# Optimization experiments

Measured on AMD Instinct MI355X. Metric: run time of the kernel, lower is better.

Reference implementation:

```python
import jax, jax.numpy as jnp
import numpy as np

EMBED_DIM = 584
HEADS = 8
HEAD_SIZE = EMBED_DIM // HEADS  # 73
CTX = 200


def setup_inputs() -> dict:
    key = jax.random.key(0)
    ks = jax.random.split(key, 6)
    B, T = 256, 200
    x = jax.random.normal(ks[0], (B, T, EMBED_DIM), dtype=jnp.float32)
    s = 1.0 / np.sqrt(EMBED_DIM)
    # per-head q/k/v Linear(EMBED_DIM, HEAD_SIZE, bias=False) weights, stacked: [H, hs, E]
    Wq = jax.random.uniform(ks[1], (HEADS, HEAD_SIZE, EMBED_DIM), jnp.float32, -s, s)
    Wk = jax.random.uniform(ks[2], (HEADS, HEAD_SIZE, EMBED_DIM), jnp.float32, -s, s)
    Wv = jax.random.uniform(ks[3], (HEADS, HEAD_SIZE, EMBED_DIM), jnp.float32, -s, s)
    Wo = jax.random.uniform(ks[4], (EMBED_DIM, EMBED_DIM), jnp.float32, -s, s)
    bo = jax.random.uniform(ks[5], (EMBED_DIM,), jnp.float32, -s, s)
    return {"x": x, "Wq": Wq, "Wk": Wk, "Wv": Wv, "Wo": Wo, "bo": bo}


def reference(x, Wq, Wk, Wv, Wo, bo):
    B, T, C = x.shape  # C == EMBED_DIM
    # per-head projections, batched: [B, H, T, hs]
    q = jnp.einsum('bte,hfe->bhtf', x, Wq)
    k = jnp.einsum('bte,hfe->bhtf', x, Wk)
    v = jnp.einsum('bte,hfe->bhtf', x, Wv)
    # NOTE: original scales by EMBED_DIM**-0.5 (C), not head_size**-0.5
    scores = jnp.einsum('bhtf,bhsf->bhts', q, k) * (C ** -0.5)
    causal = jnp.tril(jnp.ones((T, T), dtype=bool))
    scores = jnp.where(causal, scores, -jnp.inf)
    w = jax.nn.softmax(scores, axis=-1)
    out = jnp.einsum('bhts,bhsf->bhtf', w, v)  # [B,H,T,hs]
    out = out.transpose(0, 2, 1, 3).reshape(B, T, C)  # concat heads on last dim
    return out @ Wo.T + bo
```

## Files before the change

### kernel.cpp

```cpp
#include <hip/hip_runtime.h>

typedef __bf16 bf16x8 __attribute__((ext_vector_type(8)));
typedef __bf16 bf16x4 __attribute__((ext_vector_type(4)));
typedef float f32x4 __attribute__((ext_vector_type(4)));

#define EMBED 584
#define KP 608
#define HEADS 8
#define HS 73
#define HSQ 80
#define CTX 200
#define NBATCH 256
#define MROWS 51200
#define NQKV 1752

#define PSS 232

__device__ __forceinline__ void gld_lds16(__bf16* lds, const __bf16* g) {
  __builtin_amdgcn_global_load_lds(
      (const __attribute__((address_space(1))) void*)g,
      (__attribute__((address_space(3))) void*)lds, 16, 0, 0);
}

__global__ __launch_bounds__(256) void cvt_x(const float* __restrict__ x,
                                             __bf16* __restrict__ out) {
  int i = blockIdx.x * 256 + threadIdx.x;
  int r = i / 76, slot = i - r * 76;
  int col = slot * 8;
  bf16x8 o8 = {};
  if (col < EMBED) {
    const float4* s4 = (const float4*)(x + (size_t)r * EMBED + col);
    float4 f0 = s4[0], f1 = s4[1];
    o8[0] = (__bf16)f0.x; o8[1] = (__bf16)f0.y; o8[2] = (__bf16)f0.z; o8[3] = (__bf16)f0.w;
    o8[4] = (__bf16)f1.x; o8[5] = (__bf16)f1.y; o8[6] = (__bf16)f1.z; o8[7] = (__bf16)f1.w;
  }
  *(bf16x8*)(out + (size_t)r * KP + col) = o8;
}

__global__ __launch_bounds__(256) void pack_w(const float* __restrict__ Wq,
                                              const float* __restrict__ Wk,
                                              const float* __restrict__ Wv,
                                              const float* __restrict__ Wo,
                                              __bf16* __restrict__ out) {
  int i = blockIdx.x * 256 + threadIdx.x;
  if (i >= 2336 * 76) return;
  int r = i / 76, slot = i - r * 76;
  int col = slot * 8;
  bf16x8 o8 = {};
  if (col < EMBED) {
    const float* src = r < 584  ? Wq + (size_t)r * EMBED
                     : r < 1168 ? Wk + (size_t)(r - 584) * EMBED
                     : r < 1752 ? Wv + (size_t)(r - 1168) * EMBED
                                : Wo + (size_t)(r - 1752) * EMBED;
    const float4* s4 = (const float4*)(src + col);
    float4 f0 = s4[0], f1 = s4[1];
    o8[0] = (__bf16)f0.x; o8[1] = (__bf16)f0.y; o8[2] = (__bf16)f0.z; o8[3] = (__bf16)f0.w;
    o8[4] = (__bf16)f1.x; o8[5] = (__bf16)f1.y; o8[6] = (__bf16)f1.z; o8[7] = (__bf16)f1.w;
  }
  *(bf16x8*)(out + (size_t)r * KP + col) = o8;
}

__global__ __launch_bounds__(256) void zero_pads(__bf16* __restrict__ qb,
                                                 __bf16* __restrict__ kb,
                                                 __bf16* __restrict__ vb) {
  int bh = blockIdx.x;
  bf16x8 z = {};
  __bf16* qp = qb + (size_t)bh * 16000;
  __bf16* kp = kb + (size_t)bh * 16000;
  __bf16* vp = vb + (size_t)bh * 16000;
  for (int i = threadIdx.x; i < 575; i += 256) {
    if (i < 200)      *(bf16x8*)&qp[i * 80 + 72] = z;
    else if (i < 400) *(bf16x8*)&kp[(i - 200) * 80 + 72] = z;
    else              *(bf16x8*)&vp[14600 + (i - 400) * 8] = z;
  }
}

__global__ __launch_bounds__(256) void gemm_qkv(const __bf16* __restrict__ A,
                                                const __bf16* __restrict__ Bm,
                                                __bf16* __restrict__ Q,
                                                __bf16* __restrict__ Ko,
                                                __bf16* __restrict__ V) {
  __shared__ __bf16 As[3][4096];
  __shared__ __bf16 Bs[3][4096];
  int tid = threadIdx.x;
  int id = blockIdx.x;
  int idp = (id & 7) * 700 + (id >> 3);
  int bm = idp / 14, bn = idp - bm * 14;
  int wid = tid >> 6, lane = tid & 63;
  int wm = (wid & 1) * 64, wn = (wid >> 1) * 64;
  int lr = lane & 15, lq = lane >> 4;
  const __bf16* aB = A  + (size_t)(bm * 128 + wid * 32 + (lane >> 2)) * KP + (lane & 3) * 8;
  const __bf16* bB = Bm + (size_t)(bn * 128 + wid * 32 + (lane >> 2)) * KP + (lane & 3) * 8;
  f32x4 acc[4][4] = {};

#define STAGE_QKV(buf, kt)                                        \
  do {                                                            \
    int k0_ = (kt) * 32;                                          \
    gld_lds16(As[buf] + wid * 1024,       aB + k0_);              \
    gld_lds16(As[buf] + wid * 1024 + 512, aB + 16 * KP + k0_);    \
    gld_lds16(Bs[buf] + wid * 1024,       bB + k0_);              \
    gld_lds16(Bs[buf] + wid * 1024 + 512, bB + 16 * KP + k0_);    \
  } while (0)

  STAGE_QKV(0, 0);
  STAGE_QKV(1, 1);
#pragma unroll
  for (int kt = 0; kt < 19; ++kt) {
    if (kt < 18) asm volatile("s_waitcnt vmcnt(4)" ::: "memory");
    else         asm volatile("s_waitcnt vmcnt(0)" ::: "memory");
    __builtin_amdgcn_s_barrier();
    if (kt + 2 < 19) STAGE_QKV((kt + 2) % 3, kt + 2);
    const __bf16* Ac = As[kt % 3];
    const __bf16* Bc = Bs[kt % 3];
    bf16x8 af[4], bfr[4];
#pragma unroll
    for (int i = 0; i < 4; ++i)
      af[i] = *(const bf16x8*)&Ac[(wm + i * 16 + lr) * 32 + lq * 8];
#pragma unroll
    for (int j = 0; j < 4; ++j)
      bfr[j] = *(const bf16x8*)&Bc[(wn + j * 16 + lr) * 32 + lq * 8];
    __builtin_amdgcn_s_setprio(1);
#pragma unroll
    for (int i = 0; i < 4; ++i)
#pragma unroll
      for (int j = 0; j < 4; ++j)
        acc[i][j] = __builtin_amdgcn_mfma_f32_16x16x32_bf16(af[i], bfr[j], acc[i][j], 0, 0, 0);
    __builtin_amdgcn_s_setprio(0);
  }
#undef STAGE_QKV
  int whichj[4], ojv[4];
  __bf16* Pj[4];
  bool okj[4];
#pragma unroll
  for (int j = 0; j < 4; ++j) {
    int n = bn * 128 + wn + j * 16 + lr;
    okj[j] = (n < NQKV);
    int nn = okj[j] ? n : 0;
    int which = nn / EMBED;
    int rem = nn - which * EMBED;
    int hh = rem / HS;
    int f = rem - hh * HS;
    whichj[j] = which;
    ojv[j] = (which == 2) ? (hh * 16000 + f * 200) : (hh * 16000 + f);
    Pj[j] = (which == 0) ? Q : (which == 1) ? Ko : V;
  }
#pragma unroll
  for (int i = 0; i < 4; ++i) {
    int m0 = bm * 128 + wm + i * 16 + lq * 4;
    int bb = m0 / CTX;
    int tt = m0 - bb * CTX;
    int a_qk = bb * 128000 + tt * 80;
    int a_v  = bb * 128000 + tt;
#pragma unroll
    for (int j = 0; j < 4; ++j) {
      if (!okj[j]) continue;
      if (whichj[j] == 2) {
        bf16x4 v4;
#pragma unroll
        for (int r = 0; r < 4; ++r) v4[r] = (__bf16)acc[i][j][r];
        *(bf16x4*)&Pj[j][a_v + ojv[j]] = v4;
      } else {
        int base = a_qk + ojv[j];
#pragma unroll
        for (int r = 0; r < 4; ++r)
          Pj[j][base + r * 80] = (__bf16)acc[i][j][r];
      }
    }
  }
}

__global__ __launch_bounds__(256, 4) void attn_kernel(const __bf16* __restrict__ q,
                                                      const __bf16* __restrict__ k,
                                                      const __bf16* __restrict__ v,
                                                      __bf16* __restrict__ o) {
  __shared__ __align__(16) __bf16 Ps[4][16 * PSS];
  int tid = threadIdx.x;
  int bh = blockIdx.x;
  int b = bh >> 3, h = bh & 7;
  const __bf16* qg = q + (size_t)bh * 16000;
  const __bf16* kg = k + (size_t)bh * 16000;
  const __bf16* vg = v + (size_t)bh * 16000;

  if (h == 0) {
    bf16x8 z = {};
    for (int i = tid; i < CTX * 3; i += 256) {
      int t = i / 3, seg = i - t * 3;
      *(bf16x8*)&o[((size_t)(b * CTX + t)) * KP + EMBED + seg * 8] = z;
    }
  }

  int wid = tid >> 6, lane = tid & 63;
  int lr = lane & 15, g = lane >> 4;
  __bf16* Pw = Ps[wid];
  const float scale = 0.04138029443264672f;

  int sl[4];
  sl[0] = 12 - wid;
  sl[1] = (wid < 3) ? 6 + wid : 5;
  sl[2] = (wid < 3) ? 1 + wid : 4;
  sl[3] = (wid < 3) ? -1 : 0;

#pragma unroll
  for (int si = 0; si < 4; ++si) {
    int s = sl[si];
    if (s < 0) continue;
    int row0 = s * 16;
    bf16x8 qf[3];
    qf[0] = *(const bf16x8*)&qg[(size_t)(row0 + lr) * HSQ + g * 8];
    qf[1] = *(const bf16x8*)&qg[(size_t)(row0 + lr) * HSQ + 32 + g * 8];
    qf[2] = (g < 2) ? *(const bf16x8*)&qg[(size_t)(row0 + lr) * HSQ + 64 + g * 8]
                    : bf16x8{};
    float sc[13][4];
#pragma unroll
    for (int nt = 0; nt < 13; ++nt) {
      if (nt > s) continue;
      f32x4 acc = {};
#pragma unroll
      for (int kc = 0; kc < 3; ++kc) {
        bf16x8 kf = *(const bf16x8*)&kg[(size_t)(nt * 16 + lr) * HSQ + kc * 32 + g * 8];
        acc = __builtin_amdgcn_mfma_f32_16x16x32_bf16(qf[kc], kf, acc, 0, 0, 0);
      }
#pragma unroll
      for (int r = 0; r < 4; ++r) {
        float val = acc[r] * scale;
        if (nt == s && lr > g * 4 + r) val = -1e30f;
        if (nt * 16 + lr >= CTX) val = -1e30f;
        sc[nt][r] = val;
      }
    }
    float mr[4], rs[4];
#pragma unroll
    for (int r = 0; r < 4; ++r) {
      float m = -1e30f;
#pragma unroll
      for (int nt = 0; nt < 13; ++nt)
        if (nt <= s) m = fmaxf(m, sc[nt][r]);
      mr[r] = m;
    }
#pragma unroll
    for (int off = 8; off; off >>= 1)
#pragma unroll
      for (int r = 0; r < 4; ++r)
        mr[r] = fmaxf(mr[r], __shfl_xor(mr[r], off, 64));
#pragma unroll
    for (int r = 0; r < 4; ++r) {
      float ssum = 0.f;
#pragma unroll
      for (int nt = 0; nt < 13; ++nt) {
        if (nt > s) continue;
        sc[nt][r] = __expf(sc[nt][r] - mr[r]);
        ssum += sc[nt][r];
      }
      rs[r] = ssum;
    }
#pragma unroll
    for (int off = 8; off; off >>= 1)
#pragma unroll
      for (int r = 0; r < 4; ++r) rs[r] += __shfl_xor(rs[r], off, 64);
#pragma unroll
    for (int nt = 0; nt < 13; ++nt) {
      if (nt > s) continue;
#pragma unroll
      for (int r = 0; r < 4; ++r)
        Pw[(g * 4 + r) * PSS + nt * 16 + lr] = (__bf16)sc[nt][r];
    }
    if ((s & 1) == 0) {
#pragma unroll
      for (int r = 0; r < 4; ++r)
        Pw[(g * 4 + r) * PSS + (s + 1) * 16 + lr] = (__bf16)0.f;
    }
    f32x4 ov[5];
#pragma unroll
    for (int nt = 0; nt < 5; ++nt) ov[nt] = f32x4{0.f, 0.f, 0.f, 0.f};
#pragma unroll
    for (int kc = 0; kc < 7; ++kc) {
      if (kc > s / 2) continue;
      bf16x8 pf = *(const bf16x8*)&Pw[lr * PSS + kc * 32 + g * 8];
#pragma unroll
      for (int nt = 0; nt < 5; ++nt) {
        bf16x8 vf = *(const bf16x8*)&vg[(size_t)(nt * 16 + lr) * CTX + kc * 32 + g * 8];
        ov[nt] = __builtin_amdgcn_mfma_f32_16x16x32_bf16(pf, vf, ov[nt], 0, 0, 0);
      }
    }
    float inv[4];
#pragma unroll
    for (int r = 0; r < 4; ++r) inv[r] = 1.0f / rs[r];
#pragma unroll
    for (int nt = 0; nt < 5; ++nt) {
      int f = nt * 16 + lr;
      if (f < HS) {
#pragma unroll
        for (int r = 0; r < 4; ++r) {
          int t = row0 + g * 4 + r;
          if (t < CTX)
            o[((size_t)(b * CTX + t)) * KP + h * HS + f] =
                (__bf16)(ov[nt][r] * inv[r]);
        }
      }
    }
  }
}

__global__ __launch_bounds__(256) void gemm_out(const __bf16* __restrict__ A,
                                                const __bf16* __restrict__ Bm,
                                                const float* __restrict__ bias,
                                                float* __restrict__ C) {
  constexpr int N = EMBED;
  __shared__ __bf16 As[3][4096];
  __shared__ __bf16 Bs[3][4096];
  int tid = threadIdx.x;
  int id = blockIdx.x;
  int idp = (id & 7) * 250 + (id >> 3);
  int bm = idp / 5, bn = idp - bm * 5;
  int wid = tid >> 6, lane = tid & 63;
  int wm = (wid & 1) * 64, wn = (wid >> 1) * 64;
  int lr = lane & 15, lq = lane >> 4;
  const __bf16* aB = A  + (size_t)(bm * 128 + wid * 32 + (lane >> 2)) * KP + (lane & 3) * 8;
  const __bf16* bB = Bm + (size_t)(bn * 128 + wid * 32 + (lane >> 2)) * KP + (lane & 3) * 8;
  f32x4 acc[4][4] = {};

#define STAGE_OUT(buf, kt)                                        \
  do {                                                            \
    int k0_ = (kt) * 32;                                          \
    gld_lds16(As[buf] + wid * 1024,       aB + k0_);              \
    gld_lds16(As[buf] + wid * 1024 + 512, aB + 16 * KP + k0_);    \
    gld_lds16(Bs[buf] + wid * 1024,       bB + k0_);              \
    gld_lds16(Bs[buf] + wid * 1024 + 512, bB + 16 * KP + k0_);    \
  } while (0)

  STAGE_OUT(0, 0);
  STAGE_OUT(1, 1);
#pragma unroll
  for (int kt = 0; kt < 19; ++kt) {
    if (kt < 18) asm volatile("s_waitcnt vmcnt(4)" ::: "memory");
    else         asm volatile("s_waitcnt vmcnt(0)" ::: "memory");
    __builtin_amdgcn_s_barrier();
    if (kt + 2 < 19) STAGE_OUT((kt + 2) % 3, kt + 2);
    const __bf16* Ac = As[kt % 3];
    const __bf16* Bc = Bs[kt % 3];
    bf16x8 af[4], bfr[4];
#pragma unroll
    for (int i = 0; i < 4; ++i)
      af[i] = *(const bf16x8*)&Ac[(wm + i * 16 + lr) * 32 + lq * 8];
#pragma unroll
    for (int j = 0; j < 4; ++j)
      bfr[j] = *(const bf16x8*)&Bc[(wn + j * 16 + lr) * 32 + lq * 8];
    __builtin_amdgcn_s_setprio(1);
#pragma unroll
    for (int i = 0; i < 4; ++i)
#pragma unroll
      for (int j = 0; j < 4; ++j)
        acc[i][j] = __builtin_amdgcn_mfma_f32_16x16x32_bf16(af[i], bfr[j], acc[i][j], 0, 0, 0);
    __builtin_amdgcn_s_setprio(0);
  }
#undef STAGE_OUT
#pragma unroll
  for (int i = 0; i < 4; ++i) {
    int m = bm * 128 + wm + i * 16 + lq * 4;
#pragma unroll
    for (int j = 0; j < 4; ++j) {
      int n = bn * 128 + wn + j * 16 + lr;
      if (n < N) {
        float bval = bias[n];
#pragma unroll
        for (int r = 0; r < 4; ++r)
          C[(size_t)(m + r) * N + n] = acc[i][j][r] + bval;
      }
    }
  }
}

extern "C" void kernel_launch(void* const* d_in, const int* in_sizes, int n_in,
                              void* d_out, int out_size, void* d_ws, size_t ws_size,
                              hipStream_t stream) {
  const float* x  = (const float*)d_in[0];
  const float* Wq = (const float*)d_in[1];
  const float* Wk = (const float*)d_in[2];
  const float* Wv = (const float*)d_in[3];
  const float* Wo = (const float*)d_in[4];
  const float* bo = (const float*)d_in[5];
  float* out = (float*)d_out;

  __bf16* wcat = (__bf16*)d_ws;
  __bf16* vb   = wcat + 1420288ULL;
  __bf16* qb   = vb + 32768000ULL;
  __bf16* kb   = qb + 32768000ULL;
  __bf16* xb   = kb + 32768000ULL;
  __bf16* ab   = xb;

  cvt_x<<<15200, 256, 0, stream>>>(x, xb);
  pack_w<<<694, 256, 0, stream>>>(Wq, Wk, Wv, Wo, wcat);
  zero_pads<<<2048, 256, 0, stream>>>(qb, kb, vb);
  gemm_qkv<<<5600, 256, 0, stream>>>(xb, wcat, qb, kb, vb);
  attn_kernel<<<2048, 256, 0, stream>>>(qb, kb, vb, ab);
  gemm_out<<<2000, 256, 0, stream>>>(ab, wcat + 1752ULL * KP, bo, out);
}
```

Before: 654.1 us.

## Load GEMM B fragments directly to registers and swizzle double-buffered A tiles

Both bf16 GEMMs (QKV projection and output projection) no longer stage the weight operand through LDS. Each wave loads its B fragments straight from global memory into registers, one k-step ahead. The A tile goes from triple to double buffering in LDS with an XOR swizzle to reduce bank conflicts, and launch bounds now request 4 blocks per CU. The aim is lower LDS footprint and traffic and higher occupancy. The cost is redundant global loads of B across the two waves that share a column block, and a shallower prefetch for A.

```diff
diff --git a/kernel.cpp b/kernel.cpp
--- a/kernel.cpp
+++ b/kernel.cpp
@@ -75,13 +75,12 @@
   }
 }
 
-__global__ __launch_bounds__(256) void gemm_qkv(const __bf16* __restrict__ A,
-                                                const __bf16* __restrict__ Bm,
-                                                __bf16* __restrict__ Q,
-                                                __bf16* __restrict__ Ko,
-                                                __bf16* __restrict__ V) {
-  __shared__ __bf16 As[3][4096];
-  __shared__ __bf16 Bs[3][4096];
+__global__ __launch_bounds__(256, 4) void gemm_qkv(const __bf16* __restrict__ A,
+                                                   const __bf16* __restrict__ Bm,
+                                                   __bf16* __restrict__ Q,
+                                                   __bf16* __restrict__ Ko,
+                                                   __bf16* __restrict__ V) {
+  __shared__ __bf16 As[2][4096];
   int tid = threadIdx.x;
   int id = blockIdx.x;
   int idp = (id & 7) * 700 + (id >> 3);
@@ -89,36 +88,44 @@
   int wid = tid >> 6, lane = tid & 63;
   int wm = (wid & 1) * 64, wn = (wid >> 1) * 64;
   int lr = lane & 15, lq = lane >> 4;
-  const __bf16* aB = A  + (size_t)(bm * 128 + wid * 32 + (lane >> 2)) * KP + (lane & 3) * 8;
-  const __bf16* bB = Bm + (size_t)(bn * 128 + wid * 32 + (lane >> 2)) * KP + (lane & 3) * 8;
+  int sw = ((lane & 3) ^ ((lane >> 2) & 3)) * 8;
+  const __bf16* aB = A + (size_t)(bm * 128 + wid * 32 + (lane >> 2)) * KP + sw;
+  const __bf16* bp0 = Bm + (size_t)(bn * 128 + wn +  0 + lr) * KP + lq * 8;
+  const __bf16* bp1 = Bm + (size_t)(bn * 128 + wn + 16 + lr) * KP + lq * 8;
+  const __bf16* bp2 = Bm + (size_t)(bn * 128 + wn + 32 + lr) * KP + lq * 8;
+  const __bf16* bp3 = Bm + (size_t)(bn * 128 + wn + 48 + lr) * KP + lq * 8;
   f32x4 acc[4][4] = {};
-
-#define STAGE_QKV(buf, kt)                                        \
+  bf16x8 bfr[4];
+
+#define STAGE_A(buf, kt)                                          \
   do {                                                            \
     int k0_ = (kt) * 32;                                          \
     gld_lds16(As[buf] + wid * 1024,       aB + k0_);              \
     gld_lds16(As[buf] + wid * 1024 + 512, aB + 16 * KP + k0_);    \
-    gld_lds16(Bs[buf] + wid * 1024,       bB + k0_);              \
-    gld_lds16(Bs[buf] + wid * 1024 + 512, bB + 16 * KP + k0_);    \
   } while (0)
-
-  STAGE_QKV(0, 0);
-  STAGE_QKV(1, 1);
+#define LOAD_B(kt)                                                \
+  do {                                                            \
+    bfr[0] = *(const bf16x8*)(bp0 + (kt) * 32);                   \
+    bfr[1] = *(const bf16x8*)(bp1 + (kt) * 32);                   \
+    bfr[2] = *(const bf16x8*)(bp2 + (kt) * 32);                   \
+    bfr[3] = *(const bf16x8*)(bp3 + (kt) * 32);                   \
+  } while (0)
+
+  STAGE_A(0, 0);
+  LOAD_B(0);
+  int cxr = (lq ^ (lr & 3)) * 8;
 #pragma unroll
   for (int kt = 0; kt < 19; ++kt) {
-    if (kt < 18) asm volatile("s_waitcnt vmcnt(4)" ::: "memory");
+    asm volatile("s_waitcnt vmcnt(4)" ::: "memory");
+    __builtin_amdgcn_s_barrier();
+    if (kt < 18) STAGE_A((kt + 1) & 1, kt + 1);
+    const __bf16* Ac = As[kt & 1];
+    bf16x8 af[4];
+#pragma unroll
+    for (int i = 0; i < 4; ++i)
+      af[i] = *(const bf16x8*)&Ac[(wm + i * 16 + lr) * 32 + cxr];
+    if (kt < 18) asm volatile("s_waitcnt vmcnt(2)" ::: "memory");
     else         asm volatile("s_waitcnt vmcnt(0)" ::: "memory");
-    __builtin_amdgcn_s_barrier();
-    if (kt + 2 < 19) STAGE_QKV((kt + 2) % 3, kt + 2);
-    const __bf16* Ac = As[kt % 3];
-    const __bf16* Bc = Bs[kt % 3];
-    bf16x8 af[4], bfr[4];
-#pragma unroll
-    for (int i = 0; i < 4; ++i)
-      af[i] = *(const bf16x8*)&Ac[(wm + i * 16 + lr) * 32 + lq * 8];
-#pragma unroll
-    for (int j = 0; j < 4; ++j)
-      bfr[j] = *(const bf16x8*)&Bc[(wn + j * 16 + lr) * 32 + lq * 8];
     __builtin_amdgcn_s_setprio(1);
 #pragma unroll
     for (int i = 0; i < 4; ++i)
@@ -126,8 +133,10 @@
       for (int j = 0; j < 4; ++j)
         acc[i][j] = __builtin_amdgcn_mfma_f32_16x16x32_bf16(af[i], bfr[j], acc[i][j], 0, 0, 0);
     __builtin_amdgcn_s_setprio(0);
-  }
-#undef STAGE_QKV
+    if (kt < 18) LOAD_B(kt + 1);
+  }
+#undef STAGE_A
+#undef LOAD_B
   int whichj[4], ojv[4];
   __bf16* Pj[4];
   bool okj[4];
@@ -301,13 +310,12 @@
   }
 }
 
-__global__ __launch_bounds__(256) void gemm_out(const __bf16* __restrict__ A,
-                                                const __bf16* __restrict__ Bm,
-                                                const float* __restrict__ bias,
-                                                float* __restrict__ C) {
+__global__ __launch_bounds__(256, 4) void gemm_out(const __bf16* __restrict__ A,
+                                                   const __bf16* __restrict__ Bm,
+                                                   const float* __restrict__ bias,
+                                                   float* __restrict__ C) {
   constexpr int N = EMBED;
-  __shared__ __bf16 As[3][4096];
-  __shared__ __bf16 Bs[3][4096];
+  __shared__ __bf16 As[2][4096];
   int tid = threadIdx.x;
   int id = blockIdx.x;
   int idp = (id & 7) * 250 + (id >> 3);
@@ -315,36 +323,44 @@
   int wid = tid >> 6, lane = tid & 63;
   int wm = (wid & 1) * 64, wn = (wid >> 1) * 64;
   int lr = lane & 15, lq = lane >> 4;
-  const __bf16* aB = A  + (size_t)(bm * 128 + wid * 32 + (lane >> 2)) * KP + (lane & 3) * 8;
-  const __bf16* bB = Bm + (size_t)(bn * 128 + wid * 32 + (lane >> 2)) * KP + (lane & 3) * 8;
+  int sw = ((lane & 3) ^ ((lane >> 2) & 3)) * 8;
+  const __bf16* aB = A + (size_t)(bm * 128 + wid * 32 + (lane >> 2)) * KP + sw;
+  const __bf16* bp0 = Bm + (size_t)(bn * 128 + wn +  0 + lr) * KP + lq * 8;
+  const __bf16* bp1 = Bm + (size_t)(bn * 128 + wn + 16 + lr) * KP + lq * 8;
+  const __bf16* bp2 = Bm + (size_t)(bn * 128 + wn + 32 + lr) * KP + lq * 8;
+  const __bf16* bp3 = Bm + (size_t)(bn * 128 + wn + 48 + lr) * KP + lq * 8;
   f32x4 acc[4][4] = {};
-
-#define STAGE_OUT(buf, kt)                                        \
+  bf16x8 bfr[4];
+
+#define STAGE_A(buf, kt)                                          \
   do {                                                            \
     int k0_ = (kt) * 32;                                          \
     gld_lds16(As[buf] + wid * 1024,       aB + k0_);              \
     gld_lds16(As[buf] + wid * 1024 + 512, aB + 16 * KP + k0_);    \
-    gld_lds16(Bs[buf] + wid * 1024,       bB + k0_);              \
-    gld_lds16(Bs[buf] + wid * 1024 + 512, bB + 16 * KP + k0_);    \
   } while (0)
-
-  STAGE_OUT(0, 0);
-  STAGE_OUT(1, 1);
+#define LOAD_B(kt)                                                \
+  do {                                                            \
+    bfr[0] = *(const bf16x8*)(bp0 + (kt) * 32);                   \
+    bfr[1] = *(const bf16x8*)(bp1 + (kt) * 32);                   \
+    bfr[2] = *(const bf16x8*)(bp2 + (kt) * 32);                   \
+    bfr[3] = *(const bf16x8*)(bp3 + (kt) * 32);                   \
+  } while (0)
+
+  STAGE_A(0, 0);
+  LOAD_B(0);
+  int cxr = (lq ^ (lr & 3)) * 8;
 #pragma unroll
   for (int kt = 0; kt < 19; ++kt) {
-    if (kt < 18) asm volatile("s_waitcnt vmcnt(4)" ::: "memory");
+    asm volatile("s_waitcnt vmcnt(4)" ::: "memory");
+    __builtin_amdgcn_s_barrier();
+    if (kt < 18) STAGE_A((kt + 1) & 1, kt + 1);
+    const __bf16* Ac = As[kt & 1];
+    bf16x8 af[4];
+#pragma unroll
+    for (int i = 0; i < 4; ++i)
+      af[i] = *(const bf16x8*)&Ac[(wm + i * 16 + lr) * 32 + cxr];
+    if (kt < 18) asm volatile("s_waitcnt vmcnt(2)" ::: "memory");
     else         asm volatile("s_waitcnt vmcnt(0)" ::: "memory");
-    __builtin_amdgcn_s_barrier();
-    if (kt + 2 < 19) STAGE_OUT((kt + 2) % 3, kt + 2);
-    const __bf16* Ac = As[kt % 3];
-    const __bf16* Bc = Bs[kt % 3];
-    bf16x8 af[4], bfr[4];
-#pragma unroll
-    for (int i = 0; i < 4; ++i)
-      af[i] = *(const bf16x8*)&Ac[(wm + i * 16 + lr) * 32 + lq * 8];
-#pragma unroll
-    for (int j = 0; j < 4; ++j)
-      bfr[j] = *(const bf16x8*)&Bc[(wn + j * 16 + lr) * 32 + lq * 8];
     __builtin_amdgcn_s_setprio(1);
 #pragma unroll
     for (int i = 0; i < 4; ++i)
@@ -352,8 +368,10 @@
       for (int j = 0; j < 4; ++j)
         acc[i][j] = __builtin_amdgcn_mfma_f32_16x16x32_bf16(af[i], bfr[j], acc[i][j], 0, 0, 0);
     __builtin_amdgcn_s_setprio(0);
-  }
-#undef STAGE_OUT
+    if (kt < 18) LOAD_B(kt + 1);
+  }
+#undef STAGE_A
+#undef LOAD_B
 #pragma unroll
   for (int i = 0; i < 4; ++i) {
     int m = bm * 128 + wm + i * 16 + lq * 4;
```

After: 682.2 us. +4.3%, slower.
